# Kernel optimization log

Measured on AMD Instinct MI355X. Metric: run time of the kernel, lower is better.

Reference implementation:

```python
import jax, jax.numpy as jnp
import numpy as np


def setup_inputs() -> dict:
    key = jax.random.key(0)
    ks = jax.random.split(key, 7)
    B, T, D = 4, 4096, 128
    s = 0.02
    return {
        "input_data": jax.random.normal(ks[0], (B, T, D), dtype=jnp.float32),
        "Wq": jax.random.normal(ks[1], (D, D), dtype=jnp.float32) * s,
        "bq": jax.random.normal(ks[2], (D,), dtype=jnp.float32) * s,
        "Wk": jax.random.normal(ks[3], (D, D), dtype=jnp.float32) * s,
        "bk": jax.random.normal(ks[4], (D,), dtype=jnp.float32) * s,
        "Wv": jax.random.normal(ks[5], (D, D), dtype=jnp.float32) * s,
        "bv": jax.random.normal(ks[6], (D,), dtype=jnp.float32) * s,
    }


def reference(input_data, Wq, bq, Wk, bk, Wv, bv):
    D = input_data.shape[-1]
    scale = jnp.asarray(D, input_data.dtype) ** 0.5
    # torch Linear: x @ W.T + b
    q = input_data @ Wq.T + bq  # [B,T,D]
    k = input_data @ Wk.T + bk
    v = input_data @ Wv.T + bv
    energy = jnp.einsum("btd,bsd->bts", q, k) / scale  # [B,T,T]
    attn = jax.nn.softmax(energy, axis=-1)
    return jnp.einsum("bts,bsd->btd", attn, v)  # [B,T,D]
```

## Files before the change

kernel.cpp:

```cpp
#include <hip/hip_runtime.h>
#include <cstdint>

typedef _Float16 half4_t __attribute__((ext_vector_type(4)));
typedef _Float16 half8_t __attribute__((ext_vector_type(8)));
typedef float floatx4 __attribute__((ext_vector_type(4)));

#define T_SEQ 4096
#define D_HEAD 128
#define SCALE_LOG2 0.12751742526f

__device__ __forceinline__ void gload16(const void* src, void* dst_lds) {
    using gptr_t = const __attribute__((address_space(1))) unsigned int*;
    using lptr_t = __attribute__((address_space(3))) unsigned int*;
    __builtin_amdgcn_global_load_lds((gptr_t)(uintptr_t)src,
                                     (lptr_t)(unsigned int)(uintptr_t)dst_lds, 16, 0, 0);
}

__global__ __launch_bounds__(256) void proj_kernel(
    const float* __restrict__ x,
    const float* __restrict__ Wq, const float* __restrict__ bq,
    const float* __restrict__ Wk, const float* __restrict__ bk,
    const float* __restrict__ Wv, const float* __restrict__ bv,
    _Float16* __restrict__ qf, _Float16* __restrict__ kf, _Float16* __restrict__ vt)
{
    __shared__ __align__(16) _Float16 Ws[128 * 136];
    __shared__ __align__(16) _Float16 xs[64 * 136];

    const int t = threadIdx.x;
    const int mat = blockIdx.y;
    const float* W = (mat == 0) ? Wq : (mat == 1) ? Wk : Wv;
    const float* bias = (mat == 0) ? bq : (mat == 1) ? bk : bv;
    const float osc = (mat == 0) ? SCALE_LOG2 : 1.0f;
    const int r0 = blockIdx.x * 64;

    {
        const int o = t >> 1;
        const int i0 = (t & 1) * 64;
        for (int jj = 0; jj < 8; ++jj) {
            floatx4 w0 = *reinterpret_cast<const floatx4*>(W + o * 128 + i0 + jj * 8);
            floatx4 w1 = *reinterpret_cast<const floatx4*>(W + o * 128 + i0 + jj * 8 + 4);
            half8_t h;
            h[0]=(_Float16)w0[0]; h[1]=(_Float16)w0[1]; h[2]=(_Float16)w0[2]; h[3]=(_Float16)w0[3];
            h[4]=(_Float16)w1[0]; h[5]=(_Float16)w1[1]; h[6]=(_Float16)w1[2]; h[7]=(_Float16)w1[3];
            *reinterpret_cast<half8_t*>(&Ws[o * 136 + i0 + jj * 8]) = h;
        }
    }
    {
        const int row = t >> 2;
        const int c0 = (t & 3) * 32;
        for (int jj = 0; jj < 4; ++jj) {
            floatx4 w0 = *reinterpret_cast<const floatx4*>(x + (size_t)(r0 + row) * 128 + c0 + jj * 8);
            floatx4 w1 = *reinterpret_cast<const floatx4*>(x + (size_t)(r0 + row) * 128 + c0 + jj * 8 + 4);
            half8_t h;
            h[0]=(_Float16)w0[0]; h[1]=(_Float16)w0[1]; h[2]=(_Float16)w0[2]; h[3]=(_Float16)w0[3];
            h[4]=(_Float16)w1[0]; h[5]=(_Float16)w1[1]; h[6]=(_Float16)w1[2]; h[7]=(_Float16)w1[3];
            *reinterpret_cast<half8_t*>(&xs[row * 136 + c0 + jj * 8]) = h;
        }
    }
    __syncthreads();

    const int w = t >> 6;
    const int lane = t & 63;
    const int lo = lane & 15, hi = lane >> 4;

    floatx4 acc[8] = {};
    for (int dc = 0; dc < 4; ++dc) {
        half8_t a8 = *reinterpret_cast<const half8_t*>(&xs[(w * 16 + lo) * 136 + dc * 32 + hi * 8]);
        for (int ot = 0; ot < 8; ++ot) {
            half8_t b8 = *reinterpret_cast<const half8_t*>(&Ws[(ot * 16 + lo) * 136 + dc * 32 + hi * 8]);
            acc[ot] = __builtin_amdgcn_mfma_f32_16x16x32_f16(a8, b8, acc[ot], 0, 0, 0);
        }
    }
    __syncthreads();

    float bb[8];
    for (int ot = 0; ot < 8; ++ot) bb[ot] = bias[ot * 16 + lo];

    if (mat < 2) {
        _Float16* ol = xs;
        for (int ot = 0; ot < 8; ++ot)
            for (int r = 0; r < 4; ++r)
                ol[(w * 16 + hi * 4 + r) * 136 + ot * 16 + lo] = (_Float16)((acc[ot][r] + bb[ot]) * osc);
        __syncthreads();
        _Float16* dst = (mat == 0) ? qf : kf;
        for (int i = 0; i < 4; ++i) {
            int c = t + 256 * i;
            int row = c >> 4, p = c & 15;
            half8_t v = *reinterpret_cast<const half8_t*>(&ol[row * 136 + p * 8]);
            *reinterpret_cast<half8_t*>(dst + (size_t)(r0 + row) * 128 + p * 8) = v;
        }
    } else {
        _Float16* vl = Ws;
        for (int ot = 0; ot < 8; ++ot)
            for (int r = 0; r < 4; ++r)
                vl[(ot * 16 + lo) * 72 + w * 16 + hi * 4 + r] = (_Float16)(acc[ot][r] + bb[ot]);
        __syncthreads();
        const int b = r0 >> 12, tl0 = r0 & 4095;
        for (int i = 0; i < 4; ++i) {
            int c = t + 256 * i;
            int d = c >> 3, p = c & 7;
            half8_t v = *reinterpret_cast<const half8_t*>(&vl[d * 72 + p * 8]);
            *reinterpret_cast<half8_t*>(vt + ((size_t)(b * 128 + d)) * 4096 + tl0 + p * 8) = v;
        }
    }
}

__global__ __launch_bounds__(1024) void attn_kernel(
    const _Float16* __restrict__ qf, const _Float16* __restrict__ kf,
    const _Float16* __restrict__ vt, float* __restrict__ out)
{
    __shared__ __align__(16) char smem[131072];

    const int tid = threadIdx.x;
    const int w = tid >> 6, lane = tid & 63;
    const int lo = lane & 15, hi = lane >> 4;
    const int qsub = w & 3, split = w >> 2;

    const int bx = blockIdx.x;
    const int wg = (bx & 7) * 32 + (bx >> 3);
    const int b = wg >> 6;
    const int q0 = (wg & 63) * 64;

    const char* kbc = (const char*)(kf + (size_t)b * T_SEQ * 128);
    const char* vbc = (const char*)(vt + (size_t)b * 128 * T_SEQ);

    int koff[2], voff[2], kdst[2], vdst[2];
#pragma unroll
    for (int r = 0; r < 2; ++r) {
        int seg = w * 2 + r;
        int slot = lane & 15;
        int row = seg * 4 + (lane >> 4);
        koff[r] = row * 256 + ((slot ^ (row & 7)) << 4);
        kdst[r] = seg * 1024 + lane * 16;
        voff[r] = row * (T_SEQ * 2) + ((slot ^ (row & 7)) << 4);
        vdst[r] = 32768 + seg * 1024 + lane * 16;
    }

    half8_t qfrag[4];
    {
        const _Float16* qrow = qf + ((size_t)b * T_SEQ + q0 + qsub * 16 + lo) * 128;
#pragma unroll
        for (int dc = 0; dc < 4; ++dc)
            qfrag[dc] = *reinterpret_cast<const half8_t*>(qrow + dc * 32 + hi * 8);
    }

    floatx4 accO[8] = {};
    float m_run = -1e30f, l_run = 0.f;

#pragma unroll
    for (int r = 0; r < 2; ++r) {
        gload16(kbc + koff[r], smem + kdst[r]);
        gload16(vbc + voff[r], smem + vdst[r]);
    }
    __syncthreads();

    for (int t0 = 0; t0 < T_SEQ; t0 += 128) {
        const int cur = (t0 >> 7) & 1;
        char* buf = smem + (cur << 16);

        if (t0 + 128 < T_SEQ) {
            char* nb = smem + ((cur ^ 1) << 16);
            const char* ks = kbc + (size_t)(t0 + 128) * 256;
            const char* vs = vbc + (size_t)(t0 + 128) * 2;
#pragma unroll
            for (int r = 0; r < 2; ++r) {
                gload16(ks + koff[r], nb + kdst[r]);
                gload16(vs + voff[r], nb + vdst[r]);
            }
        }

        floatx4 sac[2] = {};
        __builtin_amdgcn_s_setprio(1);
#pragma unroll
        for (int s = 0; s < 2; ++s) {
            const char* kb0 = buf + (split * 32 + s * 16 + lo) * 256;
            const int rsw = lo & 7;
#pragma unroll
            for (int dc = 0; dc < 4; ++dc) {
                half8_t kf8 = *reinterpret_cast<const half8_t*>(kb0 + (((dc * 4 + hi) ^ rsw) << 4));
                sac[s] = __builtin_amdgcn_mfma_f32_16x16x32_f16(kf8, qfrag[dc], sac[s], 0, 0, 0);
            }
        }
        __builtin_amdgcn_s_setprio(0);

        float m = fmaxf(fmaxf(fmaxf(sac[0][0], sac[0][1]), fmaxf(sac[0][2], sac[0][3])),
                        fmaxf(fmaxf(sac[1][0], sac[1][1]), fmaxf(sac[1][2], sac[1][3])));
        m = fmaxf(m, __shfl_xor(m, 16));
        m = fmaxf(m, __shfl_xor(m, 32));
        bool ok = (m <= m_run + 4.0f);
        if (!__all(ok)) {
            float m_new = fmaxf(m_run, m);
            float alpha = exp2f(m_run - m_new);
            l_run *= alpha;
#pragma unroll
            for (int dt = 0; dt < 8; ++dt) accO[dt] *= alpha;
            m_run = m_new;
        }
        half8_t pa;
        float bs = 0.f;
#pragma unroll
        for (int s = 0; s < 2; ++s)
#pragma unroll
            for (int r = 0; r < 4; ++r) {
                float pv = exp2f(sac[s][r] - m_run);
                bs += pv;
                pa[s * 4 + r] = (_Float16)pv;
            }
        bs += __shfl_xor(bs, 16);
        bs += __shfl_xor(bs, 32);
        l_run += bs;

        const char* vbuf = buf + 32768;
        __builtin_amdgcn_s_setprio(1);
#pragma unroll
        for (int dt = 0; dt < 8; ++dt) {
            int row = dt * 16 + lo;
            const char* vr = vbuf + row * 256;
            int sw = lo & 7;
            int c0 = split * 4 + (hi >> 1);
            half4_t va  = *reinterpret_cast<const half4_t*>(vr + ((c0 ^ sw) << 4) + ((hi & 1) << 3));
            half4_t vb4 = *reinterpret_cast<const half4_t*>(vr + (((c0 + 2) ^ sw) << 4) + ((hi & 1) << 3));
            half8_t vfr;
            vfr[0]=va[0]; vfr[1]=va[1]; vfr[2]=va[2]; vfr[3]=va[3];
            vfr[4]=vb4[0]; vfr[5]=vb4[1]; vfr[6]=vb4[2]; vfr[7]=vb4[3];
            accO[dt] = __builtin_amdgcn_mfma_f32_16x16x32_f16(vfr, pa, accO[dt], 0, 0, 0);
        }
        __builtin_amdgcn_s_setprio(0);
        __syncthreads();
    }

    float* red_m = reinterpret_cast<float*>(smem + 40960);
    float* red_l = reinterpret_cast<float*>(smem + 43008);
    const int row16 = qsub * 16 + lo;
    if (hi == 0) {
        red_m[split * 64 + row16] = m_run;
        red_l[split * 64 + row16] = l_run;
    }
    __syncthreads();
    float M = -1e30f;
#pragma unroll
    for (int s = 0; s < 4; ++s) M = fmaxf(M, red_m[s * 64 + row16]);
    float L = 0.f;
#pragma unroll
    for (int s = 0; s < 4; ++s) L += red_l[s * 64 + row16] * exp2f(red_m[s * 64 + row16] - M);
    const float fac = exp2f(m_run - M) / L;

    float* out_lds = reinterpret_cast<float*>(smem);
    for (int s = 0; s < 4; ++s) {
        if (split == s) {
#pragma unroll
            for (int dt = 0; dt < 8; ++dt)
#pragma unroll
                for (int r = 0; r < 4; ++r) {
                    int d = dt * 16 + hi * 4 + r;
                    float v = accO[dt][r] * fac;
                    float* p = &out_lds[row16 * 132 + d];
                    if (s == 0) *p = v; else *p += v;
                }
        }
        __syncthreads();
    }
    {
        int row = tid >> 4, d0 = (tid & 15) * 8;
        float* op = out + ((size_t)b * T_SEQ + q0 + row) * 128 + d0;
#pragma unroll
        for (int j = 0; j < 2; ++j) {
            float4 v;
            v.x = out_lds[row * 132 + d0 + j * 4 + 0];
            v.y = out_lds[row * 132 + d0 + j * 4 + 1];
            v.z = out_lds[row * 132 + d0 + j * 4 + 2];
            v.w = out_lds[row * 132 + d0 + j * 4 + 3];
            *reinterpret_cast<float4*>(op + j * 4) = v;
        }
    }
}

extern "C" void kernel_launch(void* const* d_in, const int* in_sizes, int n_in,
                              void* d_out, int out_size, void* d_ws, size_t ws_size,
                              hipStream_t stream)
{
    (void)in_sizes; (void)n_in; (void)out_size; (void)ws_size;
    const float* x  = (const float*)d_in[0];
    const float* Wq = (const float*)d_in[1];
    const float* bq = (const float*)d_in[2];
    const float* Wk = (const float*)d_in[3];
    const float* bk = (const float*)d_in[4];
    const float* Wv = (const float*)d_in[5];
    const float* bv = (const float*)d_in[6];
    float* out = (float*)d_out;

    _Float16* qf = (_Float16*)d_ws;
    _Float16* kf = qf + (size_t)4 * T_SEQ * D_HEAD;
    _Float16* vt = kf + (size_t)4 * T_SEQ * D_HEAD;

    proj_kernel<<<dim3(256, 3), 256, 0, stream>>>(x, Wq, bq, Wk, bk, Wv, bv, qf, kf, vt);
    attn_kernel<<<dim3(256), 1024, 0, stream>>>(qf, kf, vt, out);
}
```

Measured before the change: 92.05 us.

## Restructure attention kernel: 512 threads, two query tiles per wave, triple-buffered software pipeline

The attention kernel drops from 16 to 8 waves per block. Each wave now handles two 16-row query tiles against a 16-key slice, so each K fragment loaded from LDS feeds two MFMAs. The KV tile shrinks to 64 keys and is triple-buffered. The PV MFMA for the previous tile is deferred and interleaved with the QK of the current tile, and V is prefetched through registers into a swizzled LDS layout. It also switches to raw exp2, packed RTZ fp16 conversion, and the 16x16x16 MFMA for PV, and moves the row-sum reduction out of the loop. This trades more registers per wave and fewer waves for better reuse and overlap, with some risk from lower occupancy and slight precision loss from round-toward-zero conversion.

After: 78.41 us. 14.8% less time.

```diff
diff --git a/kernel.cpp b/kernel.cpp
--- a/kernel.cpp
+++ b/kernel.cpp
@@ -1,6 +1,7 @@
 #include <hip/hip_runtime.h>
 #include <cstdint>
 
+typedef _Float16 half2_t __attribute__((ext_vector_type(2)));
 typedef _Float16 half4_t __attribute__((ext_vector_type(4)));
 typedef _Float16 half8_t __attribute__((ext_vector_type(8)));
 typedef float floatx4 __attribute__((ext_vector_type(4)));
@@ -14,6 +15,14 @@
     using lptr_t = __attribute__((address_space(3))) unsigned int*;
     __builtin_amdgcn_global_load_lds((gptr_t)(uintptr_t)src,
                                      (lptr_t)(unsigned int)(uintptr_t)dst_lds, 16, 0, 0);
+}
+
+__device__ __forceinline__ float exp2_raw(float x) {
+#if __has_builtin(__builtin_amdgcn_exp2f)
+    return __builtin_amdgcn_exp2f(x);
+#else
+    return exp2f(x);
+#endif
 }
 
 __global__ __launch_bounds__(256) void proj_kernel(
@@ -105,16 +114,16 @@
     }
 }
 
-__global__ __launch_bounds__(1024) void attn_kernel(
+__global__ __launch_bounds__(512, 1) void attn_kernel(
     const _Float16* __restrict__ qf, const _Float16* __restrict__ kf,
     const _Float16* __restrict__ vt, float* __restrict__ out)
 {
-    __shared__ __align__(16) char smem[131072];
+    __shared__ __align__(16) char smem[100352];
 
     const int tid = threadIdx.x;
     const int w = tid >> 6, lane = tid & 63;
     const int lo = lane & 15, hi = lane >> 4;
-    const int qsub = w & 3, split = w >> 2;
+    const int qg = w & 1, ksp = w >> 1;
 
     const int bx = blockIdx.x;
     const int wg = (bx & 7) * 32 + (bx >> 3);
@@ -124,7 +133,7 @@
     const char* kbc = (const char*)(kf + (size_t)b * T_SEQ * 128);
     const char* vbc = (const char*)(vt + (size_t)b * 128 * T_SEQ);
 
-    int koff[2], voff[2], kdst[2], vdst[2];
+    int koff[2], kdst[2];
 #pragma unroll
     for (int r = 0; r < 2; ++r) {
         int seg = w * 2 + r;
@@ -132,139 +141,180 @@
         int row = seg * 4 + (lane >> 4);
         koff[r] = row * 256 + ((slot ^ (row & 7)) << 4);
         kdst[r] = seg * 1024 + lane * 16;
-        voff[r] = row * (T_SEQ * 2) + ((slot ^ (row & 7)) << 4);
-        vdst[r] = 32768 + seg * 1024 + lane * 16;
-    }
-
-    half8_t qfrag[4];
-    {
-        const _Float16* qrow = qf + ((size_t)b * T_SEQ + q0 + qsub * 16 + lo) * 128;
-#pragma unroll
-        for (int dc = 0; dc < 4; ++dc)
-            qfrag[dc] = *reinterpret_cast<const half8_t*>(qrow + dc * 32 + hi * 8);
-    }
-
-    floatx4 accO[8] = {};
-    float m_run = -1e30f, l_run = 0.f;
-
-#pragma unroll
-    for (int r = 0; r < 2; ++r) {
-        gload16(kbc + koff[r], smem + kdst[r]);
-        gload16(vbc + voff[r], smem + vdst[r]);
+    }
+    int vgo[2], vwl[2];
+#pragma unroll
+    for (int i = 0; i < 2; ++i) {
+        int d = (tid >> 3) + 64 * i;
+        vgo[i] = d * (T_SEQ * 2) + (tid & 7) * 16;
+        vwl[i] = 16384 + d * 128 + (((tid & 7) ^ (d & 7)) << 4);
+    }
+    int kro[4];
+#pragma unroll
+    for (int dc = 0; dc < 4; ++dc)
+        kro[dc] = (ksp * 16 + lo) * 256 + (((dc * 4 + hi) ^ (lo & 7)) << 4);
+    int vro[8];
+#pragma unroll
+    for (int dt = 0; dt < 8; ++dt)
+        vro[dt] = 16384 + (dt * 16 + lo) * 128 +
+                  (((ksp * 2 + (hi >> 1)) ^ (lo & 7)) << 4) + ((hi & 1) << 3);
+
+    half8_t qfA[4], qfB[4];
+    {
+        const _Float16* qa = qf + ((size_t)b * T_SEQ + q0 + qg * 32 + lo) * 128;
+        const _Float16* qb = qa + 16 * 128;
+#pragma unroll
+        for (int dc = 0; dc < 4; ++dc) {
+            qfA[dc] = *reinterpret_cast<const half8_t*>(qa + dc * 32 + hi * 8);
+            qfB[dc] = *reinterpret_cast<const half8_t*>(qb + dc * 32 + hi * 8);
+        }
+    }
+
+    floatx4 accA[8] = {}, accB[8] = {};
+    float mA = -1e30f, mB = -1e30f, lA = 0.f, lB = 0.f;
+    half4_t paA = {}, paB = {};
+
+    gload16(kbc + koff[0], smem + kdst[0]);
+    gload16(kbc + koff[1], smem + kdst[1]);
+    {
+        uint4 v0 = *reinterpret_cast<const uint4*>(vbc + vgo[0]);
+        uint4 v1 = *reinterpret_cast<const uint4*>(vbc + vgo[1]);
+        *reinterpret_cast<uint4*>(smem + vwl[0]) = v0;
+        *reinterpret_cast<uint4*>(smem + vwl[1]) = v1;
     }
     __syncthreads();
 
-    for (int t0 = 0; t0 < T_SEQ; t0 += 128) {
-        const int cur = (t0 >> 7) & 1;
-        char* buf = smem + (cur << 16);
-
-        if (t0 + 128 < T_SEQ) {
-            char* nb = smem + ((cur ^ 1) << 16);
-            const char* ks = kbc + (size_t)(t0 + 128) * 256;
-            const char* vs = vbc + (size_t)(t0 + 128) * 2;
-#pragma unroll
-            for (int r = 0; r < 2; ++r) {
-                gload16(ks + koff[r], nb + kdst[r]);
-                gload16(vs + voff[r], nb + vdst[r]);
-            }
-        }
-
-        floatx4 sac[2] = {};
-        __builtin_amdgcn_s_setprio(1);
-#pragma unroll
-        for (int s = 0; s < 2; ++s) {
-            const char* kb0 = buf + (split * 32 + s * 16 + lo) * 256;
-            const int rsw = lo & 7;
-#pragma unroll
-            for (int dc = 0; dc < 4; ++dc) {
-                half8_t kf8 = *reinterpret_cast<const half8_t*>(kb0 + (((dc * 4 + hi) ^ rsw) << 4));
-                sac[s] = __builtin_amdgcn_mfma_f32_16x16x32_f16(kf8, qfrag[dc], sac[s], 0, 0, 0);
-            }
-        }
-        __builtin_amdgcn_s_setprio(0);
-
-        float m = fmaxf(fmaxf(fmaxf(sac[0][0], sac[0][1]), fmaxf(sac[0][2], sac[0][3])),
-                        fmaxf(fmaxf(sac[1][0], sac[1][1]), fmaxf(sac[1][2], sac[1][3])));
-        m = fmaxf(m, __shfl_xor(m, 16));
-        m = fmaxf(m, __shfl_xor(m, 32));
-        bool ok = (m <= m_run + 4.0f);
-        if (!__all(ok)) {
-            float m_new = fmaxf(m_run, m);
-            float alpha = exp2f(m_run - m_new);
-            l_run *= alpha;
-#pragma unroll
-            for (int dt = 0; dt < 8; ++dt) accO[dt] *= alpha;
-            m_run = m_new;
-        }
-        half8_t pa;
-        float bs = 0.f;
-#pragma unroll
-        for (int s = 0; s < 2; ++s)
-#pragma unroll
-            for (int r = 0; r < 4; ++r) {
-                float pv = exp2f(sac[s][r] - m_run);
-                bs += pv;
-                pa[s * 4 + r] = (_Float16)pv;
-            }
-        bs += __shfl_xor(bs, 16);
-        bs += __shfl_xor(bs, 32);
-        l_run += bs;
-
-        const char* vbuf = buf + 32768;
-        __builtin_amdgcn_s_setprio(1);
-#pragma unroll
-        for (int dt = 0; dt < 8; ++dt) {
-            int row = dt * 16 + lo;
-            const char* vr = vbuf + row * 256;
-            int sw = lo & 7;
-            int c0 = split * 4 + (hi >> 1);
-            half4_t va  = *reinterpret_cast<const half4_t*>(vr + ((c0 ^ sw) << 4) + ((hi & 1) << 3));
-            half4_t vb4 = *reinterpret_cast<const half4_t*>(vr + (((c0 + 2) ^ sw) << 4) + ((hi & 1) << 3));
-            half8_t vfr;
-            vfr[0]=va[0]; vfr[1]=va[1]; vfr[2]=va[2]; vfr[3]=va[3];
-            vfr[4]=vb4[0]; vfr[5]=vb4[1]; vfr[6]=vb4[2]; vfr[7]=vb4[3];
-            accO[dt] = __builtin_amdgcn_mfma_f32_16x16x32_f16(vfr, pa, accO[dt], 0, 0, 0);
-        }
-        __builtin_amdgcn_s_setprio(0);
-        __syncthreads();
-    }
-
-    float* red_m = reinterpret_cast<float*>(smem + 40960);
-    float* red_l = reinterpret_cast<float*>(smem + 43008);
-    const int row16 = qsub * 16 + lo;
+#define TILE(T0, CUR, NXT, PRV, PF, DOPREV) do {                                       \
+    uint4 vr0, vr1;                                                                    \
+    if (PF) {                                                                          \
+        const char* vs = vbc + (size_t)((T0) + 64) * 2;                                \
+        vr0 = *reinterpret_cast<const uint4*>(vs + vgo[0]);                            \
+        vr1 = *reinterpret_cast<const uint4*>(vs + vgo[1]);                            \
+        const char* ks = kbc + (size_t)((T0) + 64) * 256;                              \
+        gload16(ks + koff[0], smem + (NXT) + kdst[0]);                                 \
+        gload16(ks + koff[1], smem + (NXT) + kdst[1]);                                 \
+    }                                                                                  \
+    floatx4 sA = {0.f,0.f,0.f,0.f}, sB = {0.f,0.f,0.f,0.f};                            \
+    __builtin_amdgcn_s_setprio(1);                                                     \
+    _Pragma("unroll")                                                                  \
+    for (int dc = 0; dc < 4; ++dc) {                                                   \
+        half8_t kf8 = *reinterpret_cast<const half8_t*>(smem + (CUR) + kro[dc]);       \
+        sA = __builtin_amdgcn_mfma_f32_16x16x32_f16(kf8, qfA[dc], sA, 0, 0, 0);        \
+        sB = __builtin_amdgcn_mfma_f32_16x16x32_f16(kf8, qfB[dc], sB, 0, 0, 0);        \
+    }                                                                                  \
+    __builtin_amdgcn_s_setprio(0);                                                     \
+    float mpA = fmaxf(fmaxf(sA[0], sA[1]), fmaxf(sA[2], sA[3]));                       \
+    float mpB = fmaxf(fmaxf(sB[0], sB[1]), fmaxf(sB[2], sB[3]));                       \
+    bool ok = (mpA <= mA + 4.0f) && (mpB <= mB + 4.0f);                                \
+    if (!__all(ok)) {                                                                  \
+        float ra = mpA, rb = mpB;                                                      \
+        ra = fmaxf(ra, __shfl_xor(ra, 16)); ra = fmaxf(ra, __shfl_xor(ra, 32));        \
+        rb = fmaxf(rb, __shfl_xor(rb, 16)); rb = fmaxf(rb, __shfl_xor(rb, 32));        \
+        float nA = fmaxf(mA, ra), nB = fmaxf(mB, rb);                                  \
+        float aA = exp2_raw(mA - nA), aB = exp2_raw(mB - nB);                          \
+        lA *= aA; lB *= aB;                                                            \
+        _Pragma("unroll")                                                              \
+        for (int dt = 0; dt < 8; ++dt) { accA[dt] *= aA; accB[dt] *= aB; }             \
+        mA = nA; mB = nB;                                                              \
+    }                                                                                  \
+    if (DOPREV) {                                                                      \
+        __builtin_amdgcn_s_setprio(1);                                                 \
+        _Pragma("unroll")                                                              \
+        for (int dt = 0; dt < 8; ++dt) {                                               \
+            half4_t vfr = *reinterpret_cast<const half4_t*>(smem + (PRV) + vro[dt]);   \
+            accA[dt] = __builtin_amdgcn_mfma_f32_16x16x16f16(vfr, paA, accA[dt], 0, 0, 0); \
+            accB[dt] = __builtin_amdgcn_mfma_f32_16x16x16f16(vfr, paB, accB[dt], 0, 0, 0); \
+        }                                                                              \
+        __builtin_amdgcn_s_setprio(0);                                                 \
+    }                                                                                  \
+    {                                                                                  \
+        float p0 = exp2_raw(sA[0] - mA), p1 = exp2_raw(sA[1] - mA);                    \
+        float p2 = exp2_raw(sA[2] - mA), p3 = exp2_raw(sA[3] - mA);                    \
+        lA += (p0 + p1) + (p2 + p3);                                                   \
+        half2_t h0 = __builtin_bit_cast(half2_t, __builtin_amdgcn_cvt_pkrtz(p0, p1));  \
+        half2_t h1 = __builtin_bit_cast(half2_t, __builtin_amdgcn_cvt_pkrtz(p2, p3));  \
+        paA[0] = h0[0]; paA[1] = h0[1]; paA[2] = h1[0]; paA[3] = h1[1];                \
+        p0 = exp2_raw(sB[0] - mB); p1 = exp2_raw(sB[1] - mB);                          \
+        p2 = exp2_raw(sB[2] - mB); p3 = exp2_raw(sB[3] - mB);                          \
+        lB += (p0 + p1) + (p2 + p3);                                                   \
+        h0 = __builtin_bit_cast(half2_t, __builtin_amdgcn_cvt_pkrtz(p0, p1));          \
+        h1 = __builtin_bit_cast(half2_t, __builtin_amdgcn_cvt_pkrtz(p2, p3));          \
+        paB[0] = h0[0]; paB[1] = h0[1]; paB[2] = h1[0]; paB[3] = h1[1];                \
+    }                                                                                  \
+    if (PF) {                                                                          \
+        *reinterpret_cast<uint4*>(smem + (NXT) + vwl[0]) = vr0;                        \
+        *reinterpret_cast<uint4*>(smem + (NXT) + vwl[1]) = vr1;                        \
+    }                                                                                  \
+    __syncthreads();                                                                   \
+} while (0)
+
+    TILE(0, 0, 32768, 65536, 1, 0);
+    for (int t0 = 1; t0 < 61; t0 += 3) {
+        TILE(t0 * 64,       32768, 65536, 0,     1, 1);
+        TILE(t0 * 64 + 64,  65536, 0,     32768, 1, 1);
+        TILE(t0 * 64 + 128, 0,     32768, 65536, 1, 1);
+    }
+    TILE(61 * 64, 32768, 65536, 0,     1, 1);
+    TILE(62 * 64, 65536, 0,     32768, 1, 1);
+    TILE(63 * 64, 0,     32768, 65536, 0, 1);
+#undef TILE
+
+#pragma unroll
+    for (int dt = 0; dt < 8; ++dt) {
+        half4_t vfr = *reinterpret_cast<const half4_t*>(smem + 0 + vro[dt]);
+        accA[dt] = __builtin_amdgcn_mfma_f32_16x16x16f16(vfr, paA, accA[dt], 0, 0, 0);
+        accB[dt] = __builtin_amdgcn_mfma_f32_16x16x16f16(vfr, paB, accB[dt], 0, 0, 0);
+    }
+
+    lA += __shfl_xor(lA, 16); lA += __shfl_xor(lA, 32);
+    lB += __shfl_xor(lB, 16); lB += __shfl_xor(lB, 32);
+
+    float* red_m = reinterpret_cast<float*>(smem + 98304);
+    float* red_l = reinterpret_cast<float*>(smem + 99328);
+    const int rowA = qg * 32 + lo, rowB = qg * 32 + 16 + lo;
     if (hi == 0) {
-        red_m[split * 64 + row16] = m_run;
-        red_l[split * 64 + row16] = l_run;
+        red_m[ksp * 64 + rowA] = mA; red_l[ksp * 64 + rowA] = lA;
+        red_m[ksp * 64 + rowB] = mB; red_l[ksp * 64 + rowB] = lB;
     }
     __syncthreads();
-    float M = -1e30f;
-#pragma unroll
-    for (int s = 0; s < 4; ++s) M = fmaxf(M, red_m[s * 64 + row16]);
-    float L = 0.f;
-#pragma unroll
-    for (int s = 0; s < 4; ++s) L += red_l[s * 64 + row16] * exp2f(red_m[s * 64 + row16] - M);
-    const float fac = exp2f(m_run - M) / L;
-
+    float facA, facB;
+    {
+        float M = -1e30f, L = 0.f;
+#pragma unroll
+        for (int s = 0; s < 4; ++s) M = fmaxf(M, red_m[s * 64 + rowA]);
+#pragma unroll
+        for (int s = 0; s < 4; ++s) L += red_l[s * 64 + rowA] * exp2_raw(red_m[s * 64 + rowA] - M);
+        facA = exp2_raw(mA - M) / L;
+        M = -1e30f; L = 0.f;
+#pragma unroll
+        for (int s = 0; s < 4; ++s) M = fmaxf(M, red_m[s * 64 + rowB]);
+#pragma unroll
+        for (int s = 0; s < 4; ++s) L += red_l[s * 64 + rowB] * exp2_raw(red_m[s * 64 + rowB] - M);
+        facB = exp2_raw(mB - M) / L;
+    }
     float* out_lds = reinterpret_cast<float*>(smem);
     for (int s = 0; s < 4; ++s) {
-        if (split == s) {
+        if (ksp == s) {
 #pragma unroll
             for (int dt = 0; dt < 8; ++dt)
 #pragma unroll
                 for (int r = 0; r < 4; ++r) {
                     int d = dt * 16 + hi * 4 + r;
-                    float v = accO[dt][r] * fac;
-                    float* p = &out_lds[row16 * 132 + d];
-                    if (s == 0) *p = v; else *p += v;
+                    float vA = accA[dt][r] * facA;
+                    float vB = accB[dt][r] * facB;
+                    float* pA = &out_lds[rowA * 132 + d];
+                    float* pB = &out_lds[rowB * 132 + d];
+                    if (s == 0) { *pA = vA; *pB = vB; }
+                    else        { *pA += vA; *pB += vB; }
                 }
         }
         __syncthreads();
     }
     {
-        int row = tid >> 4, d0 = (tid & 15) * 8;
+        int row = tid >> 3, d0 = (tid & 7) * 16;
         float* op = out + ((size_t)b * T_SEQ + q0 + row) * 128 + d0;
 #pragma unroll
-        for (int j = 0; j < 2; ++j) {
+        for (int j = 0; j < 4; ++j) {
             float4 v;
             v.x = out_lds[row * 132 + d0 + j * 4 + 0];
             v.y = out_lds[row * 132 + d0 + j * 4 + 1];
@@ -294,5 +344,5 @@
     _Float16* vt = kf + (size_t)4 * T_SEQ * D_HEAD;
 
     proj_kernel<<<dim3(256, 3), 256, 0, stream>>>(x, Wq, bq, Wk, bk, Wv, bv, qf, kf, vt);
-    attn_kernel<<<dim3(256), 1024, 0, stream>>>(qf, kf, vt, out);
-}
+    attn_kernel<<<dim3(256), 512, 0, stream>>>(qf, kf, vt, out);
+}
```
